# Optimization experiments

Measured on AMD Instinct MI355X. Metric: run time of the kernel, lower is better.

The kernel has to match this reference:

```python
import jax, jax.numpy as jnp
import numpy as np

N_NODES = 100000


def _gcn_norm(edge_index, n):
    # PyG GCNConv default: add self-loops, symmetric normalization
    src, dst = edge_index[0], edge_index[1]
    loops = jnp.arange(n, dtype=src.dtype)
    src = jnp.concatenate([src, loops])
    dst = jnp.concatenate([dst, loops])
    deg = jax.ops.segment_sum(jnp.ones_like(dst, dtype=jnp.float32), dst, num_segments=n)
    dinv = jnp.where(deg > 0, jax.lax.rsqrt(deg), 0.0)
    norm = dinv[src] * dinv[dst]  # [E+N]
    return src, dst, norm


def _gcn_conv(x, src, dst, norm, W, b, n):
    h = x @ W                                  # [N, out] transform first
    msg = h[src] * norm[:, None]               # gather + edge weight
    out = jax.ops.segment_sum(msg, dst, num_segments=n)  # scatter-add
    return out + b


def setup_inputs() -> dict:
    key = jax.random.key(0)
    k1, k2, k3, k4 = jax.random.split(key, 4)
    in_f, h_f, out_f = 128, 256, 128
    x = jax.random.normal(k1, (N_NODES, in_f), dtype=jnp.float32)
    edge_index = jax.random.randint(k2, (2, 1600000), 0, N_NODES, dtype=jnp.int64)
    W1 = jax.random.normal(k3, (in_f, h_f), dtype=jnp.float32) / np.sqrt(in_f)
    b1 = jnp.zeros((h_f,), dtype=jnp.float32)
    W2 = jax.random.normal(k4, (h_f, out_f), dtype=jnp.float32) / np.sqrt(h_f)
    b2 = jnp.zeros((out_f,), dtype=jnp.float32)
    return {"x": x, "edge_index": edge_index, "W1": W1, "b1": b1, "W2": W2, "b2": b2}


def reference(x, edge_index, W1, b1, W2, b2):
    n = x.shape[0]
    src, dst, norm = _gcn_norm(edge_index, n)
    h = jax.nn.relu(_gcn_conv(x, src, dst, norm, W1, b1, n))
    return _gcn_conv(h, src, dst, norm, W2, b2, n)
```

## Files before the change

### kernel.cpp

```cpp
#include <hip/hip_runtime.h>

typedef __bf16 bf16x8 __attribute__((ext_vector_type(8)));
typedef float f32x4 __attribute__((ext_vector_type(4)));

#define DEVI static __device__ __forceinline__
#define CHUNK 4096

DEVI unsigned short f2bf(float f){
  unsigned int x = __builtin_bit_cast(unsigned int, f);
  x = (x + 0x7fffu + ((x >> 16) & 1u)) >> 16;
  return (unsigned short)x;
}
DEVI unsigned int packbf2(float a, float b){
  return (unsigned int)f2bf(a) | ((unsigned int)f2bf(b) << 16);
}
DEVI float bflo(unsigned int u){ return __builtin_bit_cast(float, u << 16); }
DEVI float bfhi(unsigned int u){ return __builtin_bit_cast(float, u & 0xffff0000u); }

__global__ void k_zero(int* __restrict__ p, int n){
  int i = blockIdx.x*256 + threadIdx.x;
  if (i < n) p[i] = 0;
}


__global__ __launch_bounds__(256) void kb_hist(const int* __restrict__ dst,
    int* __restrict__ bucketCnt, int E, int NB){
  __shared__ int h[2048];
  for (int i=threadIdx.x;i<NB;i+=256) h[i]=0;
  __syncthreads();
  int base = blockIdx.x*CHUNK;
  int lim = base+CHUNK < E ? base+CHUNK : E;
  for (int i = base+threadIdx.x; i < lim; i += 256)
    atomicAdd(&h[dst[i]>>8], 1);
  __syncthreads();
  for (int i=threadIdx.x;i<NB;i+=256)
    if (h[i]) atomicAdd(&bucketCnt[i], h[i]);
}

__global__ __launch_bounds__(256) void kb_scan(const int* __restrict__ bucketCnt,
    int* __restrict__ bucketOff, int* __restrict__ bucketCur, int NB){
  __shared__ int sh[256];
  int t = threadIdx.x;
  int per = (NB+255)/256;
  int vals[8];
  int lsum = 0;
  for (int j=0;j<per;j++){
    int i = t*per+j;
    int v = (i<NB) ? bucketCnt[i] : 0;
    vals[j]=v; lsum+=v;
  }
  sh[t]=lsum; __syncthreads();
  for (int off=1; off<256; off<<=1){
    int x = (t>=off) ? sh[t-off] : 0;
    __syncthreads();
    sh[t] += x;
    __syncthreads();
  }
  int run = sh[t]-lsum;
  for (int j=0;j<per;j++){
    int i = t*per+j;
    if (i<NB){ bucketOff[i]=run; bucketCur[i]=run; }
    run += vals[j];
  }
  if (t==255) bucketOff[NB]=run;
}

__global__ __launch_bounds__(256) void kb_scatter(const int* __restrict__ src,
    const int* __restrict__ dst, int* __restrict__ bucketCur,
    int* __restrict__ srcb, int* __restrict__ dstb, int E, int NB){
  __shared__ int h[2048];
  __shared__ int baseSh[2048];
  for (int i=threadIdx.x;i<NB;i+=256) h[i]=0;
  __syncthreads();
  int base = blockIdx.x*CHUNK;
  int lim = base+CHUNK < E ? base+CHUNK : E;
  for (int i = base+threadIdx.x; i < lim; i += 256)
    atomicAdd(&h[dst[i]>>8], 1);
  __syncthreads();
  for (int i=threadIdx.x;i<NB;i+=256){
    int c = h[i];
    baseSh[i] = c ? atomicAdd(&bucketCur[i], c) : 0;
    h[i] = 0;
  }
  __syncthreads();
  for (int i = base+threadIdx.x; i < lim; i += 256){
    int d = dst[i];
    int b = d>>8;
    int r = atomicAdd(&h[b], 1);
    int p = baseSh[b] + r;
    srcb[p] = src[i];
    dstb[p] = d;
  }
}

__global__ __launch_bounds__(256) void kb_fused(const int* __restrict__ srcb,
    const int* __restrict__ dstb, const int* __restrict__ bOff,
    int* __restrict__ rp, int* __restrict__ csr, float* __restrict__ dinv,
    int n, int NB, int E){
  __shared__ int c[256];
  __shared__ int sh[256];
  __shared__ int cur[256];
  int t = threadIdx.x;
  int b = blockIdx.x;
  int s = bOff[b], e2 = bOff[b+1];
  c[t]=0; __syncthreads();
  for (int i=s+t;i<e2;i+=256) atomicAdd(&c[dstb[i]&255], 1);
  __syncthreads();
  int deg = c[t];
  sh[t]=deg; __syncthreads();
  for (int o=1;o<256;o<<=1){
    int x = (t>=o) ? sh[t-o] : 0;
    __syncthreads();
    sh[t]+=x;
    __syncthreads();
  }
  int excl = sh[t]-deg;
  int node = b*256+t;
  if (node<n){
    rp[node] = s + excl;
    dinv[node] = rsqrtf((float)(deg+1));
  }
  if (b==NB-1 && t==0) rp[n] = E;
  cur[t] = s + excl;
  __syncthreads();
  for (int i=s+t;i<e2;i+=256){
    int d = dstb[i]&255;
    int r = atomicAdd(&cur[d], 1);
    csr[r] = srcb[i] << 8;
  }
}

__global__ void k_cvt(const float2* __restrict__ x, const float* __restrict__ dinv,
                      unsigned int* __restrict__ xb, int n2){
  int i = blockIdx.x*256 + threadIdx.x;
  if (i<n2){
    float d = dinv[i>>6];
    float2 v = x[i];
    xb[i] = packbf2(d*v.x, d*v.y);
  }
}

DEVI void packW(const float* __restrict__ W, unsigned short* __restrict__ Wp,
                int idx, int N, int NF){
  int l = idx & 63;
  int frag = idx >> 6;
  int cf = frag % NF;
  int ks = frag / NF;
  int kbase = ks*32 + (l>>4)*8;
  int col = cf*16 + (l&15);
  unsigned short* dp = Wp + (size_t)idx*8;
  #pragma unroll
  for (int j=0;j<8;j++) dp[j] = f2bf(W[(size_t)(kbase+j)*N + col]);
}

__global__ void k_pack2(const float* __restrict__ W1, unsigned short* __restrict__ W1p,
                        const float* __restrict__ W2, unsigned short* __restrict__ W2p){
  int idx = blockIdx.x*256 + threadIdx.x;
  if (idx < 4096) packW(W1, W1p, idx, 256, 16);
  else            packW(W2, W2p, idx-4096, 128, 8);
}

#define ACC8(V) { a0+=bflo(V.x); a1+=bfhi(V.x); a2+=bflo(V.y); a3+=bfhi(V.y); \
                  a4+=bflo(V.z); a5+=bfhi(V.z); a6+=bflo(V.w); a7+=bfhi(V.w); }

template<bool FINAL>
__global__ __launch_bounds__(256) void k_agg(
    const unsigned int* __restrict__ xs, const int* __restrict__ rp,
    const int* __restrict__ csr, const float* __restrict__ dinv,
    const float* __restrict__ bias, unsigned int* __restrict__ outb,
    float* __restrict__ outf, int n){
  int node = blockIdx.x*4 + (threadIdx.x>>6);
  if (node >= n) return;
  int l = threadIdx.x & 63;
  int q = l & 15;
  int h = l >> 4;
  const char* xbase = (const char*)xs;
  float a0=0,a1=0,a2=0,a3=0,a4=0,a5=0,a6=0,a7=0;
  int e = rp[node], end = rp[node+1];
  int p = e;
  int nf = (end - e) >> 4;
  for (int blk=0; blk<nf; ++blk, p+=16){
    uint4 v[4];
    #pragma unroll
    for (int i=0;i<4;i++){
      int boff = csr[p + 4*i + h];
      v[i] = *(const uint4*)(xbase + (size_t)(unsigned)boff + q*16);
    }
    ACC8(v[0]); ACC8(v[1]); ACC8(v[2]); ACC8(v[3]);
  }
  int rem = end - p;
  if (rem >= 8){
    uint4 v[2];
    #pragma unroll
    for (int i=0;i<2;i++){
      int boff = csr[p + 4*i + h];
      v[i] = *(const uint4*)(xbase + (size_t)(unsigned)boff + q*16);
    }
    ACC8(v[0]); ACC8(v[1]);
    p += 8; rem -= 8;
  }
  if (rem > 0){
    uint4 v[2];
    #pragma unroll
    for (int i=0;i<2;i++){
      int ei = p + 4*i + h;
      int ec = ei < end-1 ? ei : end-1;
      int boff = csr[ec];
      uint4 t = *(const uint4*)(xbase + (size_t)(unsigned)boff + q*16);
      if (ei >= end){ t.x=0; t.y=0; t.z=0; t.w=0; }
      v[i] = t;
    }
    ACC8(v[0]); ACC8(v[1]);
  }
  a0 += __shfl_xor(a0,16); a0 += __shfl_xor(a0,32);
  a1 += __shfl_xor(a1,16); a1 += __shfl_xor(a1,32);
  a2 += __shfl_xor(a2,16); a2 += __shfl_xor(a2,32);
  a3 += __shfl_xor(a3,16); a3 += __shfl_xor(a3,32);
  a4 += __shfl_xor(a4,16); a4 += __shfl_xor(a4,32);
  a5 += __shfl_xor(a5,16); a5 += __shfl_xor(a5,32);
  a6 += __shfl_xor(a6,16); a6 += __shfl_xor(a6,32);
  a7 += __shfl_xor(a7,16); a7 += __shfl_xor(a7,32);
  uint4 sv = *(const uint4*)(xbase + (size_t)node*256 + q*16);
  ACC8(sv);
  float dn = dinv[node];
  if constexpr (FINAL){
    if (h < 2){
      const float4 bb = *(const float4*)(bias + 8*q + 4*h);
      float4 r;
      r.x = (h ? a4 : a0)*dn + bb.x;
      r.y = (h ? a5 : a1)*dn + bb.y;
      r.z = (h ? a6 : a2)*dn + bb.z;
      r.w = (h ? a7 : a3)*dn + bb.w;
      *(float4*)(outf + (size_t)node*128 + 8*q + 4*h) = r;
    }
  } else {
    if (h == 0){
      uint4 o;
      o.x = packbf2(a0*dn, a1*dn);
      o.y = packbf2(a2*dn, a3*dn);
      o.z = packbf2(a4*dn, a5*dn);
      o.w = packbf2(a6*dn, a7*dn);
      *(uint4*)((char*)outb + (size_t)node*256 + q*16) = o;
    }
  }
}

template<int K, int N, bool BIASRELU, bool ROWSCALE>
__global__ __launch_bounds__(256) void k_gemm(
    const unsigned short* __restrict__ A, const unsigned short* __restrict__ Wp,
    const float* __restrict__ bias, const float* __restrict__ rowscale,
    unsigned short* __restrict__ C, int M){
  constexpr int KS = K/32;
  constexpr int NF = N/16;
  constexpr int NWC = N/64;
  constexpr int NWR = 4/NWC;
  constexpr int BM = 64*NWR;
  int l = threadIdx.x & 63;
  int w = threadIdx.x >> 6;
  int wr = w / NWC, wc = w % NWC;
  int r0 = blockIdx.x*BM + wr*64;
  int c0 = wc*64;
  int lr = l & 15, lg = l >> 4;
  f32x4 acc[4][4];
  #pragma unroll
  for (int i=0;i<4;i++)
    #pragma unroll
    for (int j=0;j<4;j++)
      acc[i][j] = f32x4{0.f,0.f,0.f,0.f};
  for (int ks=0; ks<KS; ++ks){
    bf16x8 a[4], b[4];
    #pragma unroll
    for (int ar=0;ar<4;ar++){
      int row = r0 + ar*16 + lr;
      if (row > M-1) row = M-1;
      const uint4* p = (const uint4*)(A + (size_t)row*K + ks*32 + lg*8);
      union { uint4 u; bf16x8 v; } t; t.u = *p; a[ar] = t.v;
    }
    #pragma unroll
    for (int cb=0;cb<4;cb++){
      int cf = (c0>>4) + cb;
      const uint4* p = (const uint4*)(Wp + ((size_t)(ks*NF + cf)*64 + l)*8);
      union { uint4 u; bf16x8 v; } t; t.u = *p; b[cb] = t.v;
    }
    #pragma unroll
    for (int ar=0;ar<4;ar++)
      #pragma unroll
      for (int cb=0;cb<4;cb++)
        acc[ar][cb] = __builtin_amdgcn_mfma_f32_16x16x32_bf16(a[ar], b[cb], acc[ar][cb], 0, 0, 0);
  }
  #pragma unroll
  for (int ar=0;ar<4;ar++){
    #pragma unroll
    for (int i=0;i<4;i++){
      int row = r0 + ar*16 + lg*4 + i;
      if (row < M){
        float rs = 1.f;
        if constexpr (ROWSCALE) rs = rowscale[row];
        #pragma unroll
        for (int cb=0;cb<4;cb++){
          int col = c0 + cb*16 + lr;
          float v = acc[ar][cb][i];
          if constexpr (BIASRELU){ v += bias[col]; v = fmaxf(v, 0.f); }
          if constexpr (ROWSCALE) v *= rs;
          C[(size_t)row*N + col] = f2bf(v);
        }
      }
    }
  }
}

extern "C" void kernel_launch(void* const* d_in, const int* in_sizes, int n_in,
                              void* d_out, int out_size, void* d_ws, size_t ws_size,
                              hipStream_t stream){
  const float* x  = (const float*)d_in[0];
  const int*   ei = (const int*)d_in[1];
  const float* W1 = (const float*)d_in[2];
  const float* b1 = (const float*)d_in[3];
  const float* W2 = (const float*)d_in[4];
  const float* b2 = (const float*)d_in[5];
  const int IN_F = 128, H_F = 256, OUT_F = 128;
  int n = in_sizes[0] / IN_F;
  int E = in_sizes[1] / 2;
  const int* srcI = ei;
  const int* dstI = ei + E;
  const int NB = (n+255)>>8;

  char* ws = (char*)d_ws;
  size_t off = 0;
  auto alloc = [&](size_t bytes)->char*{
    char* p = ws + off; off += (bytes + 255) & ~(size_t)255; return p;
  };
  int*   rp    = (int*)  alloc(((size_t)n+1)*4);
  float* dinv  = (float*)alloc((size_t)n*4);
  int*   bCnt  = (int*)  alloc((size_t)NB*4);
  int*   bOff  = (int*)  alloc(((size_t)NB+1)*4);
  int*   bCur  = (int*)  alloc((size_t)NB*4);
  unsigned short* W1p = (unsigned short*)alloc((size_t)IN_F*H_F*2);
  unsigned short* W2p = (unsigned short*)alloc((size_t)H_F*OUT_F*2);
  int*   csr   = (int*)  alloc((size_t)E*4);
  unsigned int* xb = (unsigned int*)alloc((size_t)n*(IN_F/2)*4);
  unsigned int* AX = (unsigned int*)alloc((size_t)n*(IN_F/2)*4);
  unsigned short* H1 = (unsigned short*)alloc((size_t)n*H_F*2);
  int* srcb = (int*)H1;
  int* dstb = srcb + E;

  int NCH = (E + CHUNK - 1)/CHUNK;

  k_zero<<<(NB+255)/256,256,0,stream>>>(bCnt, NB);
  kb_hist<<<NCH,256,0,stream>>>(dstI, bCnt, E, NB);
  kb_scan<<<1,256,0,stream>>>(bCnt, bOff, bCur, NB);
  kb_scatter<<<NCH,256,0,stream>>>(srcI, dstI, bCur, srcb, dstb, E, NB);
  kb_fused<<<NB,256,0,stream>>>(srcb, dstb, bOff, rp, csr, dinv, n, NB, E);
  k_cvt<<<((n*(IN_F/2))+255)/256,256,0,stream>>>((const float2*)x, dinv, xb, n*(IN_F/2));
  k_pack2<<<32,256,0,stream>>>(W1, W1p, W2, W2p);
  k_agg<false><<<(n+3)/4,256,0,stream>>>(xb, rp, csr, dinv, nullptr, AX, nullptr, n);
  k_gemm<128,256,true,false><<<(n+63)/64,256,0,stream>>>((const unsigned short*)AX, W1p, b1, nullptr, H1, n);
  unsigned int* T = xb;
  k_gemm<256,128,false,true><<<(n+127)/128,256,0,stream>>>(H1, W2p, nullptr, dinv, (unsigned short*)T, n);
  k_agg<true><<<(n+3)/4,256,0,stream>>>(T, rp, csr, dinv, b2, nullptr, (float*)d_out, n);
}
```

Before: 282.1 us.

## Slice feature matrices into 16-column panels for cache-local gather aggregation

Node features feeding the two aggregation passes are stored as eight column slices of 32 bytes per node. Each aggregation block handles one slice, and blockIdx is interleaved so the eight slices of the same nodes run together. The intent is to shrink the randomly gathered working set per slice so it fits better in L2/MALL, and the CSR offsets are rescaled to match. The GEMMs read and write the sliced layout. Each wave now does 8x more gather iterations with 4-byte loads instead of 16-byte loads, and the edge index list is reread eight times. The bucket scatter kernel also moves to 1024-thread blocks over larger chunks.

```diff
diff --git a/kernel.cpp b/kernel.cpp
--- a/kernel.cpp
+++ b/kernel.cpp
@@ -5,6 +5,7 @@
 
 #define DEVI static __device__ __forceinline__
 #define CHUNK 4096
+#define SCHUNK 8192
 
 DEVI unsigned short f2bf(float f){
   unsigned int x = __builtin_bit_cast(unsigned int, f);
@@ -65,25 +66,26 @@
   if (t==255) bucketOff[NB]=run;
 }
 
-__global__ __launch_bounds__(256) void kb_scatter(const int* __restrict__ src,
+__global__ __launch_bounds__(1024) void kb_scatter(const int* __restrict__ src,
     const int* __restrict__ dst, int* __restrict__ bucketCur,
     int* __restrict__ srcb, int* __restrict__ dstb, int E, int NB){
   __shared__ int h[2048];
   __shared__ int baseSh[2048];
-  for (int i=threadIdx.x;i<NB;i+=256) h[i]=0;
-  __syncthreads();
-  int base = blockIdx.x*CHUNK;
-  int lim = base+CHUNK < E ? base+CHUNK : E;
-  for (int i = base+threadIdx.x; i < lim; i += 256)
+  int t = threadIdx.x;
+  for (int i=t;i<NB;i+=1024) h[i]=0;
+  __syncthreads();
+  int base = blockIdx.x*SCHUNK;
+  int lim = base+SCHUNK < E ? base+SCHUNK : E;
+  for (int i = base+t; i < lim; i += 1024)
     atomicAdd(&h[dst[i]>>8], 1);
   __syncthreads();
-  for (int i=threadIdx.x;i<NB;i+=256){
+  for (int i=t;i<NB;i+=1024){
     int c = h[i];
     baseSh[i] = c ? atomicAdd(&bucketCur[i], c) : 0;
     h[i] = 0;
   }
   __syncthreads();
-  for (int i = base+threadIdx.x; i < lim; i += 256){
+  for (int i = base+t; i < lim; i += 1024){
     int d = dst[i];
     int b = d>>8;
     int r = atomicAdd(&h[b], 1);
@@ -126,17 +128,21 @@
   for (int i=s+t;i<e2;i+=256){
     int d = dstb[i]&255;
     int r = atomicAdd(&cur[d], 1);
-    csr[r] = srcb[i] << 8;
+    csr[r] = srcb[i] << 5;
   }
 }
 
 __global__ void k_cvt(const float2* __restrict__ x, const float* __restrict__ dinv,
-                      unsigned int* __restrict__ xb, int n2){
+                      unsigned int* __restrict__ xb, int n, int n2){
   int i = blockIdx.x*256 + threadIdx.x;
   if (i<n2){
-    float d = dinv[i>>6];
+    int node = i>>6;
+    int fp = i&63;
+    float d = dinv[node];
     float2 v = x[i];
-    xb[i] = packbf2(d*v.x, d*v.y);
+    int sl = fp >> 3;
+    int off = fp & 7;
+    xb[((size_t)sl*n + node)*8 + off] = packbf2(d*v.x, d*v.y);
   }
 }
 
@@ -160,92 +166,48 @@
   else            packW(W2, W2p, idx-4096, 128, 8);
 }
 
-#define ACC8(V) { a0+=bflo(V.x); a1+=bfhi(V.x); a2+=bflo(V.y); a3+=bfhi(V.y); \
-                  a4+=bflo(V.z); a5+=bfhi(V.z); a6+=bflo(V.w); a7+=bfhi(V.w); }
-
 template<bool FINAL>
 __global__ __launch_bounds__(256) void k_agg(
     const unsigned int* __restrict__ xs, const int* __restrict__ rp,
     const int* __restrict__ csr, const float* __restrict__ dinv,
     const float* __restrict__ bias, unsigned int* __restrict__ outb,
     float* __restrict__ outf, int n){
-  int node = blockIdx.x*4 + (threadIdx.x>>6);
+  int bid = blockIdx.x;
+  int sl = bid & 7;
+  int node = (bid >> 3)*4 + (threadIdx.x >> 6);
   if (node >= n) return;
   int l = threadIdx.x & 63;
-  int q = l & 15;
-  int h = l >> 4;
-  const char* xbase = (const char*)xs;
-  float a0=0,a1=0,a2=0,a3=0,a4=0,a5=0,a6=0,a7=0;
+  int fl = l & 7;
+  int slot = l >> 3;
+  const char* sbase = (const char*)xs + (size_t)sl * n * 32;
+  float a0 = 0.f, a1 = 0.f;
   int e = rp[node], end = rp[node+1];
-  int p = e;
-  int nf = (end - e) >> 4;
-  for (int blk=0; blk<nf; ++blk, p+=16){
-    uint4 v[4];
-    #pragma unroll
-    for (int i=0;i<4;i++){
-      int boff = csr[p + 4*i + h];
-      v[i] = *(const uint4*)(xbase + (size_t)(unsigned)boff + q*16);
+  for (int p = e; p < end; p += 8){
+    int ei = p + slot;
+    int ec = ei < end-1 ? ei : end-1;
+    int boff = __builtin_nontemporal_load(csr + ec);
+    unsigned int v = *(const unsigned int*)(sbase + (size_t)(unsigned)boff + fl*4);
+    if (ei >= end) v = 0;
+    a0 += bflo(v); a1 += bfhi(v);
+  }
+  a0 += __shfl_xor(a0, 8); a1 += __shfl_xor(a1, 8);
+  a0 += __shfl_xor(a0,16); a1 += __shfl_xor(a1,16);
+  a0 += __shfl_xor(a0,32); a1 += __shfl_xor(a1,32);
+  if (l < 8){
+    unsigned int sv = *(const unsigned int*)(sbase + (size_t)node*32 + l*4);
+    a0 += bflo(sv); a1 += bfhi(sv);
+    float dn = dinv[node];
+    if constexpr (FINAL){
+      float2 bb = *(const float2*)(bias + sl*16 + 2*l);
+      float2 r; r.x = a0*dn + bb.x; r.y = a1*dn + bb.y;
+      *(float2*)(outf + (size_t)node*128 + sl*16 + 2*l) = r;
+    } else {
+      outb[((size_t)sl*n + node)*8 + l] = packbf2(a0*dn, a1*dn);
     }
-    ACC8(v[0]); ACC8(v[1]); ACC8(v[2]); ACC8(v[3]);
-  }
-  int rem = end - p;
-  if (rem >= 8){
-    uint4 v[2];
-    #pragma unroll
-    for (int i=0;i<2;i++){
-      int boff = csr[p + 4*i + h];
-      v[i] = *(const uint4*)(xbase + (size_t)(unsigned)boff + q*16);
-    }
-    ACC8(v[0]); ACC8(v[1]);
-    p += 8; rem -= 8;
-  }
-  if (rem > 0){
-    uint4 v[2];
-    #pragma unroll
-    for (int i=0;i<2;i++){
-      int ei = p + 4*i + h;
-      int ec = ei < end-1 ? ei : end-1;
-      int boff = csr[ec];
-      uint4 t = *(const uint4*)(xbase + (size_t)(unsigned)boff + q*16);
-      if (ei >= end){ t.x=0; t.y=0; t.z=0; t.w=0; }
-      v[i] = t;
-    }
-    ACC8(v[0]); ACC8(v[1]);
-  }
-  a0 += __shfl_xor(a0,16); a0 += __shfl_xor(a0,32);
-  a1 += __shfl_xor(a1,16); a1 += __shfl_xor(a1,32);
-  a2 += __shfl_xor(a2,16); a2 += __shfl_xor(a2,32);
-  a3 += __shfl_xor(a3,16); a3 += __shfl_xor(a3,32);
-  a4 += __shfl_xor(a4,16); a4 += __shfl_xor(a4,32);
-  a5 += __shfl_xor(a5,16); a5 += __shfl_xor(a5,32);
-  a6 += __shfl_xor(a6,16); a6 += __shfl_xor(a6,32);
-  a7 += __shfl_xor(a7,16); a7 += __shfl_xor(a7,32);
-  uint4 sv = *(const uint4*)(xbase + (size_t)node*256 + q*16);
-  ACC8(sv);
-  float dn = dinv[node];
-  if constexpr (FINAL){
-    if (h < 2){
-      const float4 bb = *(const float4*)(bias + 8*q + 4*h);
-      float4 r;
-      r.x = (h ? a4 : a0)*dn + bb.x;
-      r.y = (h ? a5 : a1)*dn + bb.y;
-      r.z = (h ? a6 : a2)*dn + bb.z;
-      r.w = (h ? a7 : a3)*dn + bb.w;
-      *(float4*)(outf + (size_t)node*128 + 8*q + 4*h) = r;
-    }
-  } else {
-    if (h == 0){
-      uint4 o;
-      o.x = packbf2(a0*dn, a1*dn);
-      o.y = packbf2(a2*dn, a3*dn);
-      o.z = packbf2(a4*dn, a5*dn);
-      o.w = packbf2(a6*dn, a7*dn);
-      *(uint4*)((char*)outb + (size_t)node*256 + q*16) = o;
-    }
-  }
-}
-
-template<int K, int N, bool BIASRELU, bool ROWSCALE>
+  }
+}
+
+template<int K, int N, bool BIASRELU, bool ROWSCALE, bool ASLICED, bool CSLICED>
 __global__ __launch_bounds__(256) void k_gemm(
     const unsigned short* __restrict__ A, const unsigned short* __restrict__ Wp,
     const float* __restrict__ bias, const float* __restrict__ rowscale,
@@ -273,7 +235,13 @@
     for (int ar=0;ar<4;ar++){
       int row = r0 + ar*16 + lr;
       if (row > M-1) row = M-1;
-      const uint4* p = (const uint4*)(A + (size_t)row*K + ks*32 + lg*8);
+      const uint4* p;
+      if constexpr (ASLICED){
+        int s2 = 2*ks + (lg>>1);
+        p = (const uint4*)((const char*)A + ((size_t)s2*M + row)*32 + (lg&1)*16);
+      } else {
+        p = (const uint4*)(A + (size_t)row*K + ks*32 + lg*8);
+      }
       union { uint4 u; bf16x8 v; } t; t.u = *p; a[ar] = t.v;
     }
     #pragma unroll
@@ -302,7 +270,11 @@
           float v = acc[ar][cb][i];
           if constexpr (BIASRELU){ v += bias[col]; v = fmaxf(v, 0.f); }
           if constexpr (ROWSCALE) v *= rs;
-          C[(size_t)row*N + col] = f2bf(v);
+          if constexpr (CSLICED){
+            C[((size_t)(col>>4)*M + row)*16 + lr] = f2bf(v);
+          } else {
+            C[(size_t)row*N + col] = f2bf(v);
+          }
         }
       }
     }
@@ -345,17 +317,18 @@
   int* dstb = srcb + E;
 
   int NCH = (E + CHUNK - 1)/CHUNK;
+  int NSC = (E + SCHUNK - 1)/SCHUNK;
 
   k_zero<<<(NB+255)/256,256,0,stream>>>(bCnt, NB);
   kb_hist<<<NCH,256,0,stream>>>(dstI, bCnt, E, NB);
   kb_scan<<<1,256,0,stream>>>(bCnt, bOff, bCur, NB);
-  kb_scatter<<<NCH,256,0,stream>>>(srcI, dstI, bCur, srcb, dstb, E, NB);
+  kb_scatter<<<NSC,1024,0,stream>>>(srcI, dstI, bCur, srcb, dstb, E, NB);
   kb_fused<<<NB,256,0,stream>>>(srcb, dstb, bOff, rp, csr, dinv, n, NB, E);
-  k_cvt<<<((n*(IN_F/2))+255)/256,256,0,stream>>>((const float2*)x, dinv, xb, n*(IN_F/2));
+  k_cvt<<<((n*(IN_F/2))+255)/256,256,0,stream>>>((const float2*)x, dinv, xb, n, n*(IN_F/2));
   k_pack2<<<32,256,0,stream>>>(W1, W1p, W2, W2p);
-  k_agg<false><<<(n+3)/4,256,0,stream>>>(xb, rp, csr, dinv, nullptr, AX, nullptr, n);
-  k_gemm<128,256,true,false><<<(n+63)/64,256,0,stream>>>((const unsigned short*)AX, W1p, b1, nullptr, H1, n);
+  k_agg<false><<<((n+3)/4)*8,256,0,stream>>>(xb, rp, csr, dinv, nullptr, AX, nullptr, n);
+  k_gemm<128,256,true,false,true,false><<<(n+63)/64,256,0,stream>>>((const unsigned short*)AX, W1p, b1, nullptr, H1, n);
   unsigned int* T = xb;
-  k_gemm<256,128,false,true><<<(n+127)/128,256,0,stream>>>(H1, W2p, nullptr, dinv, (unsigned short*)T, n);
-  k_agg<true><<<(n+3)/4,256,0,stream>>>(T, rp, csr, dinv, b2, nullptr, (float*)d_out, n);
-}
+  k_gemm<256,128,false,true,false,true><<<(n+127)/128,256,0,stream>>>(H1, W2p, nullptr, dinv, (unsigned short*)T, n);
+  k_agg<true><<<((n+3)/4)*8,256,0,stream>>>(T, rp, csr, dinv, b2, nullptr, (float*)d_out, n);
+}
```

Result: slower. 714.1 us (+153.2%).

## Split edge bucket scatter into two radix passes and add nontemporal hints

Applied to the files above, without the earlier changes.

The single-pass scatter of edges into 256-node buckets becomes a two-pass radix-style scatter. The first pass scatters into coarse 2048-node buckets, using cursors seeded in the scan kernel. The second pass scatters each coarse group into fine buckets, so each block's writes stay in a small region, improving write coalescing. This costs an extra read and write of the edge arrays plus one more launch. Separately, the aggregation kernel reads CSR indices with nontemporal loads and writes the final output with nontemporal stores to reduce cache pollution.

```diff
diff --git a/kernel.cpp b/kernel.cpp
--- a/kernel.cpp
+++ b/kernel.cpp
@@ -5,6 +5,7 @@
 
 #define DEVI static __device__ __forceinline__
 #define CHUNK 4096
+#define SCH 8192
 
 DEVI unsigned short f2bf(float f){
   unsigned int x = __builtin_bit_cast(unsigned int, f);
@@ -38,7 +39,8 @@
 }
 
 __global__ __launch_bounds__(256) void kb_scan(const int* __restrict__ bucketCnt,
-    int* __restrict__ bucketOff, int* __restrict__ bucketCur, int NB){
+    int* __restrict__ bucketOff, int* __restrict__ bucketCur,
+    int* __restrict__ cCur, int NB, int NBC){
   __shared__ int sh[256];
   int t = threadIdx.x;
   int per = (NB+255)/256;
@@ -63,33 +65,40 @@
     run += vals[j];
   }
   if (t==255) bucketOff[NB]=run;
-}
-
-__global__ __launch_bounds__(256) void kb_scatter(const int* __restrict__ src,
-    const int* __restrict__ dst, int* __restrict__ bucketCur,
-    int* __restrict__ srcb, int* __restrict__ dstb, int E, int NB){
+  __syncthreads();
+  for (int c=t;c<NBC;c+=256){
+    int f = c*8;
+    cCur[c] = bucketOff[f < NB ? f : NB];
+  }
+}
+
+template<int SHIFT>
+__global__ __launch_bounds__(512) void kb_scat(const int* __restrict__ src,
+    const int* __restrict__ dst, int* __restrict__ cur,
+    int* __restrict__ srco, int* __restrict__ dsto, int E, int NBK){
   __shared__ int h[2048];
   __shared__ int baseSh[2048];
-  for (int i=threadIdx.x;i<NB;i+=256) h[i]=0;
-  __syncthreads();
-  int base = blockIdx.x*CHUNK;
-  int lim = base+CHUNK < E ? base+CHUNK : E;
-  for (int i = base+threadIdx.x; i < lim; i += 256)
-    atomicAdd(&h[dst[i]>>8], 1);
-  __syncthreads();
-  for (int i=threadIdx.x;i<NB;i+=256){
+  int t = threadIdx.x;
+  for (int i=t;i<NBK;i+=512) h[i]=0;
+  __syncthreads();
+  int base = blockIdx.x*SCH;
+  int lim = base+SCH < E ? base+SCH : E;
+  for (int i = base+t; i < lim; i += 512)
+    atomicAdd(&h[dst[i]>>SHIFT], 1);
+  __syncthreads();
+  for (int i=t;i<NBK;i+=512){
     int c = h[i];
-    baseSh[i] = c ? atomicAdd(&bucketCur[i], c) : 0;
+    baseSh[i] = c ? atomicAdd(&cur[i], c) : 0;
     h[i] = 0;
   }
   __syncthreads();
-  for (int i = base+threadIdx.x; i < lim; i += 256){
+  for (int i = base+t; i < lim; i += 512){
     int d = dst[i];
-    int b = d>>8;
+    int b = d>>SHIFT;
     int r = atomicAdd(&h[b], 1);
     int p = baseSh[b] + r;
-    srcb[p] = src[i];
-    dstb[p] = d;
+    srco[p] = src[i];
+    dsto[p] = d;
   }
 }
 
@@ -183,7 +192,7 @@
     uint4 v[4];
     #pragma unroll
     for (int i=0;i<4;i++){
-      int boff = csr[p + 4*i + h];
+      int boff = __builtin_nontemporal_load(csr + p + 4*i + h);
       v[i] = *(const uint4*)(xbase + (size_t)(unsigned)boff + q*16);
     }
     ACC8(v[0]); ACC8(v[1]); ACC8(v[2]); ACC8(v[3]);
@@ -193,7 +202,7 @@
     uint4 v[2];
     #pragma unroll
     for (int i=0;i<2;i++){
-      int boff = csr[p + 4*i + h];
+      int boff = __builtin_nontemporal_load(csr + p + 4*i + h);
       v[i] = *(const uint4*)(xbase + (size_t)(unsigned)boff + q*16);
     }
     ACC8(v[0]); ACC8(v[1]);
@@ -205,7 +214,7 @@
     for (int i=0;i<2;i++){
       int ei = p + 4*i + h;
       int ec = ei < end-1 ? ei : end-1;
-      int boff = csr[ec];
+      int boff = __builtin_nontemporal_load(csr + ec);
       uint4 t = *(const uint4*)(xbase + (size_t)(unsigned)boff + q*16);
       if (ei >= end){ t.x=0; t.y=0; t.z=0; t.w=0; }
       v[i] = t;
@@ -226,12 +235,12 @@
   if constexpr (FINAL){
     if (h < 2){
       const float4 bb = *(const float4*)(bias + 8*q + 4*h);
-      float4 r;
+      f32x4 r;
       r.x = (h ? a4 : a0)*dn + bb.x;
       r.y = (h ? a5 : a1)*dn + bb.y;
       r.z = (h ? a6 : a2)*dn + bb.z;
       r.w = (h ? a7 : a3)*dn + bb.w;
-      *(float4*)(outf + (size_t)node*128 + 8*q + 4*h) = r;
+      __builtin_nontemporal_store(r, (f32x4*)(outf + (size_t)node*128 + 8*q + 4*h));
     }
   } else {
     if (h == 0){
@@ -323,7 +332,8 @@
   int E = in_sizes[1] / 2;
   const int* srcI = ei;
   const int* dstI = ei + E;
-  const int NB = (n+255)>>8;
+  const int NB  = (n+255)>>8;
+  const int NBC = (n+2047)>>11;
 
   char* ws = (char*)d_ws;
   size_t off = 0;
@@ -335,6 +345,7 @@
   int*   bCnt  = (int*)  alloc((size_t)NB*4);
   int*   bOff  = (int*)  alloc(((size_t)NB+1)*4);
   int*   bCur  = (int*)  alloc((size_t)NB*4);
+  int*   cCur  = (int*)  alloc(((size_t)NBC+1)*4);
   unsigned short* W1p = (unsigned short*)alloc((size_t)IN_F*H_F*2);
   unsigned short* W2p = (unsigned short*)alloc((size_t)H_F*OUT_F*2);
   int*   csr   = (int*)  alloc((size_t)E*4);
@@ -343,13 +354,17 @@
   unsigned short* H1 = (unsigned short*)alloc((size_t)n*H_F*2);
   int* srcb = (int*)H1;
   int* dstb = srcb + E;
+  int* srcc = dstb + E;
+  int* dstc = srcc + E;
 
   int NCH = (E + CHUNK - 1)/CHUNK;
+  int NSC = (E + SCH - 1)/SCH;
 
   k_zero<<<(NB+255)/256,256,0,stream>>>(bCnt, NB);
   kb_hist<<<NCH,256,0,stream>>>(dstI, bCnt, E, NB);
-  kb_scan<<<1,256,0,stream>>>(bCnt, bOff, bCur, NB);
-  kb_scatter<<<NCH,256,0,stream>>>(srcI, dstI, bCur, srcb, dstb, E, NB);
+  kb_scan<<<1,256,0,stream>>>(bCnt, bOff, bCur, cCur, NB, NBC);
+  kb_scat<11><<<NSC,512,0,stream>>>(srcI, dstI, cCur, srcc, dstc, E, NBC);
+  kb_scat<8><<<NSC,512,0,stream>>>(srcc, dstc, bCur, srcb, dstb, E, NB);
   kb_fused<<<NB,256,0,stream>>>(srcb, dstb, bOff, rp, csr, dinv, n, NB, E);
   k_cvt<<<((n*(IN_F/2))+255)/256,256,0,stream>>>((const float2*)x, dinv, xb, n*(IN_F/2));
   k_pack2<<<32,256,0,stream>>>(W1, W1p, W2, W2p);
```

Measured after the change: 293.1 us. +3.9%, slower.
